# Kernel tuning notes

Measured on AMD Instinct MI355X. Metric: run time of the kernel, lower is better.

Reference implementation:

```python
import jax, jax.numpy as jnp
import numpy as np

H = 64
L = 3
NG = 1024
# node types: 0 user, 1 card, 2 transaction, 3 merchant, 4 location, 5 device
N_NODES = [100000, 150000, 500000, 20000, 5000, 50000]
N_TX = N_NODES[2]
FEAT_DIMS = [8, 6, 12, 6, 5, 5]
NAMES = ["user", "card", "transaction", "merchant", "location", "device"]
# relation r -> (src_type, dst_type); order matches the HeteroConv dict:
# owns, made, at, in, using, followed_by, owned_by, made_with, receives, has, used_in, preceded
REL = [(0, 1), (1, 2), (2, 3), (2, 4), (2, 5), (2, 2), (1, 0), (2, 1), (3, 2), (4, 2), (5, 2), (2, 2)]
E_CNT = [150000, 500000, 500000, 500000, 500000, 500000, 150000, 500000, 500000, 500000, 500000, 500000]


def gat_conv(x_src, x_dst, src, dst, W, a_s, a_d, b, n_dst):
    # PyG GATConv, heads=1, shared src/dst linear (int in_channels), no self-loops (bipartite hetero)
    xs = x_src @ W  # [Ns, H]
    xd = x_dst @ W  # [Nd, H]
    e = jax.nn.leaky_relu((xs @ a_s)[src] + (xd @ a_d)[dst], 0.2)  # [E]
    m = jax.ops.segment_max(e, dst, num_segments=n_dst)
    m = jnp.where(jnp.isfinite(m), m, 0.0)
    p = jnp.exp(e - m[dst])
    s = jax.ops.segment_sum(p, dst, num_segments=n_dst)
    alpha = p / (s[dst] + 1e-16)
    out = jax.ops.segment_sum(alpha[:, None] * xs[src], dst, num_segments=n_dst)
    return out + b


def setup_inputs():
    key = jax.random.key(0)
    ks = iter(jax.random.split(key, 80))
    inp = {}
    for n, d, nm in zip(N_NODES, FEAT_DIMS, NAMES):
        inp["x_" + nm] = jax.random.normal(next(ks), (n, d), jnp.float32)
    for d, nm in zip(FEAT_DIMS, NAMES):
        inp["emb_" + nm + "_W"] = (jax.random.normal(next(ks), (d, H), jnp.float32) / np.sqrt(d)).astype(jnp.float32)
        inp["emb_" + nm + "_b"] = jnp.zeros((H,), jnp.float32)
    inp["gat_W"] = (jax.random.normal(next(ks), (L, 12, H, H), jnp.float32) / np.sqrt(H)).astype(jnp.float32)
    inp["gat_a_src"] = jax.random.normal(next(ks), (L, 12, H), jnp.float32) * 0.1
    inp["gat_a_dst"] = jax.random.normal(next(ks), (L, 12, H), jnp.float32) * 0.1
    inp["gat_b"] = jnp.zeros((L, 12, H), jnp.float32)
    inp["pool_W"] = (jax.random.normal(next(ks), (2 * H, H), jnp.float32) / np.sqrt(2 * H)).astype(jnp.float32)
    inp["pool_b"] = jnp.zeros((H,), jnp.float32)
    inp["cls_W1"] = (jax.random.normal(next(ks), (H, H), jnp.float32) / np.sqrt(H)).astype(jnp.float32)
    inp["cls_b1"] = jnp.zeros((H,), jnp.float32)
    inp["cls_W2"] = (jax.random.normal(next(ks), (H, 1), jnp.float32) / np.sqrt(H)).astype(jnp.float32)
    inp["cls_b2"] = jnp.zeros((1,), jnp.float32)
    for r, (s, d) in enumerate(REL):
        inp[f"e{r}_src"] = jax.random.randint(next(ks), (E_CNT[r],), 0, N_NODES[s])
        inp[f"e{r}_dst"] = jax.random.randint(next(ks), (E_CNT[r],), 0, N_NODES[d])
    inp["batch"] = jnp.sort(jax.random.randint(next(ks), (N_TX,), 0, NG))
    return inp


def reference(x_user, x_card, x_transaction, x_merchant, x_location, x_device,
              emb_user_W, emb_user_b, emb_card_W, emb_card_b,
              emb_transaction_W, emb_transaction_b, emb_merchant_W, emb_merchant_b,
              emb_location_W, emb_location_b, emb_device_W, emb_device_b,
              gat_W, gat_a_src, gat_a_dst, gat_b,
              pool_W, pool_b, cls_W1, cls_b1, cls_W2, cls_b2,
              e0_src, e0_dst, e1_src, e1_dst, e2_src, e2_dst, e3_src, e3_dst,
              e4_src, e4_dst, e5_src, e5_dst, e6_src, e6_dst, e7_src, e7_dst,
              e8_src, e8_dst, e9_src, e9_dst, e10_src, e10_dst, e11_src, e11_dst,
              batch):
    edges = [(e0_src, e0_dst), (e1_src, e1_dst), (e2_src, e2_dst), (e3_src, e3_dst),
             (e4_src, e4_dst), (e5_src, e5_dst), (e6_src, e6_dst), (e7_src, e7_dst),
             (e8_src, e8_dst), (e9_src, e9_dst), (e10_src, e10_dst), (e11_src, e11_dst)]
    x = [x_user @ emb_user_W + emb_user_b,
         x_card @ emb_card_W + emb_card_b,
         x_transaction @ emb_transaction_W + emb_transaction_b,
         x_merchant @ emb_merchant_W + emb_merchant_b,
         x_location @ emb_location_W + emb_location_b,
         x_device @ emb_device_W + emb_device_b]
    for l in range(L):
        agg = [jnp.zeros((n, H), x[0].dtype) for n in N_NODES]
        for r, (s, d) in enumerate(REL):  # HeteroConv default aggr='sum'
            agg[d] = agg[d] + gat_conv(x[s], x[d], edges[r][0], edges[r][1],
                                       gat_W[l, r], gat_a_src[l, r], gat_a_dst[l, r],
                                       gat_b[l, r], N_NODES[d])
        x = [jax.nn.relu(a) for a in agg]  # dropout(p=0.2) is identity in eval mode
    tx = x[2]
    cnt = jax.ops.segment_sum(jnp.ones((N_TX,), tx.dtype), batch, num_segments=NG)
    mean_pool = jax.ops.segment_sum(tx, batch, num_segments=NG) / jnp.maximum(cnt, 1.0)[:, None]
    max_pool = jax.ops.segment_max(tx, batch, num_segments=NG)
    max_pool = jnp.where(jnp.isfinite(max_pool), max_pool, 0.0)
    pooled = jnp.concatenate([mean_pool, max_pool], axis=1) @ pool_W + pool_b
    h = jax.nn.relu(tx @ cls_W1 + cls_b1)
    fraud_scores = jax.nn.sigmoid(h @ cls_W2 + cls_b2)
    return fraud_scores, pooled
```

## Files before the change

### kernel.cpp

```cpp
#include <hip/hip_runtime.h>
#include <hip/hip_bf16.h>

typedef unsigned int u32;
typedef unsigned short u16;
typedef _Float16 f16;
typedef float f32x4 __attribute__((ext_vector_type(4)));
typedef short bf16x8 __attribute__((ext_vector_type(8)));

#define CDIV(a,b) (((a)+(b)-1)/(b))

__device__ __forceinline__ float bf2f(u32 h){ return __uint_as_float(h<<16); }
__device__ __forceinline__ u16 f2bf(float f){
  u32 u=__float_as_uint(f);
  return (u16)((u + 0x7fffu + ((u>>16)&1u))>>16);
}
__device__ __forceinline__ void unpack8(const u16* p, float* xr){
  uint4 v=*(const uint4*)p;
  xr[0]=bf2f(v.x&0xffffu); xr[1]=bf2f(v.x>>16);
  xr[2]=bf2f(v.y&0xffffu); xr[3]=bf2f(v.y>>16);
  xr[4]=bf2f(v.z&0xffffu); xr[5]=bf2f(v.z>>16);
  xr[6]=bf2f(v.w&0xffffu); xr[7]=bf2f(v.w>>16);
}
__device__ __forceinline__ int iclamp(int i, int n){
  unsigned u=(unsigned)i; return (u>=(unsigned)n)?0:i;
}

struct EdgeTab {
  const int* dst[12];
  const int* src[12];
  int seo[13];
  int rpo[13];
  int nd[12];
  int ns[12];
};

struct GTab {
  int nn[6]; int xo[6];
  int rst[12];
  int aso[12], ado[12], rpo[12], seo[12];
  int tord[6]; int bofs[7];
  int abofs[7];
  int nrel[6], rel[6][6];
  int nrole[6]; int rwv[6][12]; int rofs[6][12];
  int dszb;
};

__global__ void kdiag(float* out, int n, float v){
  int i=blockIdx.x*blockDim.x+threadIdx.x;
  if(i<n) out[i]=(i==0)?v:0.f;
}
__global__ void kzeroi(int* p, int n){
  int i=blockIdx.x*blockDim.x+threadIdx.x;
  if(i<n) p[i]=0;
}
__global__ void kbsum(const float* __restrict__ gb, float* __restrict__ bsum){
  int l=blockIdx.x/6, t=blockIdx.x%6, j=threadIdx.x;
  const int rd[12]={1,2,3,4,5,2,0,1,2,2,2,2};
  float a=0.f;
  #pragma unroll
  for(int r=0;r<12;++r) if(rd[r]==t) a += gb[(l*12+r)*64 + j];
  bsum[(l*6+t)*64 + j]=a;
}
__global__ void kwconv(const float* __restrict__ gw, u16* __restrict__ wt, int total){
  int o=blockIdx.x*blockDim.x+threadIdx.x;
  if(o>=total) return;
  int m=o>>12, rem=o&4095, j=rem>>6, k=rem&63;
  wt[o]=f2bf(gw[(m<<12)+(k<<6)+j]);
}
__global__ void kwv(const float* __restrict__ gw, const float* __restrict__ gas,
                    const float* __restrict__ gad, float* __restrict__ wv){
  int m=blockIdx.x;
  int lr=m>>1, role=m&1;
  int k=threadIdx.x;
  const float* a=(role?gad:gas)+(size_t)lr*64;
  const float* W=gw+(size_t)lr*4096;
  float acc=0.f;
  for(int j=0;j<64;++j) acc += W[k*64+j]*a[j];
  wv[(size_t)m*64+k]=acc;
}

__global__ void khistAll(EdgeTab et, int* __restrict__ RP, int Etot){
  int i=blockIdx.x*blockDim.x+threadIdx.x;
  if(i>=Etot) return;
  int r=0;
  #pragma unroll
  for(int k=1;k<12;++k) r += (i>=et.seo[k]) ? 1 : 0;
  int e=i-et.seo[r];
  int d=iclamp(et.dst[r][e], et.nd[r]);
  atomicAdd(RP+et.rpo[r]+d,1);
}
__global__ void kscan1(const int* __restrict__ hist, int* __restrict__ rp, int* __restrict__ bsum, int N){
  __shared__ int lds[256];
  __shared__ int pref[256];
  int b=blockIdx.x, t=threadIdx.x;
  int base=b*4096+t*16;
  int v[16]; int s=0;
  #pragma unroll
  for(int k=0;k<16;++k){ int idx=base+k; v[k]=(idx<N)?hist[idx]:0; s+=v[k]; }
  lds[t]=s; __syncthreads();
  if(t==0){ int run=0; for(int i=0;i<256;++i){ pref[i]=run; run+=lds[i]; } bsum[b]=run; }
  __syncthreads();
  int run=pref[t];
  #pragma unroll
  for(int k=0;k<16;++k){ int idx=base+k; if(idx<N) rp[idx]=run; run+=v[k]; }
}
__global__ void kscan2b(int* bsum, int nb){
  __shared__ int lds[256], pref[256], tot;
  int t=threadIdx.x;
  int v[4]; int s=0;
  #pragma unroll
  for(int k=0;k<4;++k){ int idx=t*4+k; v[k]=(idx<nb)?bsum[idx]:0; s+=v[k]; }
  lds[t]=s; __syncthreads();
  if(t==0){ int run=0; for(int i=0;i<256;++i){ pref[i]=run; run+=lds[i]; } tot=run; }
  __syncthreads();
  int run=pref[t];
  #pragma unroll
  for(int k=0;k<4;++k){ int idx=t*4+k; if(idx<nb){ int x=v[k]; bsum[idx]=run; run+=x; } }
  if(t==0) bsum[nb]=tot;
}
__global__ void kscan3(int* __restrict__ rp, const int* __restrict__ bsum, int N){
  int i=blockIdx.x*blockDim.x+threadIdx.x;
  if(i<N) rp[i]+=bsum[i>>12];
}
__global__ void kscatterAll(EdgeTab et, int* __restrict__ RP, int* __restrict__ SRCS, int Etot){
  int i=blockIdx.x*blockDim.x+threadIdx.x;
  if(i>=Etot) return;
  int r=0;
  #pragma unroll
  for(int k=1;k<12;++k) r += (i>=et.seo[k]) ? 1 : 0;
  int e=i-et.seo[r];
  int d=iclamp(et.dst[r][e], et.nd[r]);
  int pos=atomicAdd(RP+et.rpo[r]+d,1);
  SRCS[pos]=iclamp(et.src[r][e], et.ns[r]);
}

template<int D>
__global__ void kemb(const float* __restrict__ xin, const float* __restrict__ W,
                     const float* __restrict__ b, u16* __restrict__ xout, int N){
  int n=blockIdx.x*blockDim.x+threadIdx.x;
  if(n>=N) return;
  float xr[D];
  #pragma unroll
  for(int k=0;k<D;++k) xr[k]=xin[(long)n*D+k];
  u16* orow=xout+(long)n*64;
  for(int j0=0;j0<64;j0+=8){
    float acc[8];
    #pragma unroll
    for(int jj=0;jj<8;++jj){
      float a=b[j0+jj];
      #pragma unroll
      for(int k=0;k<D;++k) a += xr[k]*W[k*64+j0+jj];
      acc[jj]=a;
    }
    uint4 pk;
    pk.x=(u32)f2bf(acc[0])|((u32)f2bf(acc[1])<<16);
    pk.y=(u32)f2bf(acc[2])|((u32)f2bf(acc[3])<<16);
    pk.z=(u32)f2bf(acc[4])|((u32)f2bf(acc[5])<<16);
    pk.w=(u32)f2bf(acc[6])|((u32)f2bf(acc[7])<<16);
    *(uint4*)(orow+j0)=pk;
  }
}

__global__ void kalphaM(const u16* __restrict__ X, const float* __restrict__ WVl,
                        f16* __restrict__ AA, GTab tab){
  __shared__ float wv[12*64];
  int b=blockIdx.x, tid=threadIdx.x;
  int ti=0;
  #pragma unroll
  for(int k=1;k<6;++k) ti += (b>=tab.abofs[k]) ? 1 : 0;
  int t=tab.tord[ti];
  int nr=tab.nrole[t];
  for(int i=tid;i<nr*64;i+=256){
    int ro=i>>6, j=i&63;
    wv[i]=WVl[tab.rwv[t][ro]*64+j];
  }
  __syncthreads();
  int nid=(b-tab.abofs[ti])*256+tid;
  if(nid>=tab.nn[t]) return;
  const u16* row=X+((long)tab.xo[t]+nid)*64;
  float xr[64];
  #pragma unroll
  for(int j=0;j<64;j+=8) unpack8(row+j,xr+j);
  for(int ro=0;ro<nr;++ro){
    float acc=0.f;
    #pragma unroll
    for(int k=0;k<64;++k) acc += xr[k]*wv[ro*64+k];
    AA[tab.rofs[t][ro]+nid]=(f16)acc;
  }
}

#define LZ 0
#define LW 8192
#define LC 16384
__global__ void kfusedM2(const u16* __restrict__ Xc, u16* __restrict__ Xn,
                         const u16* __restrict__ WTl, const f16* __restrict__ AA,
                         const int* __restrict__ RP, const int* __restrict__ SRCS,
                         const float* __restrict__ BSl, GTab tab){
  __shared__ char L[32768];
  int tid=threadIdx.x;
  int b=blockIdx.x;
  int ti=0;
  #pragma unroll
  for(int k=1;k<6;++k) ti += (b>=tab.bofs[k]) ? 1 : 0;
  int t=tab.tord[ti];
  int d0=(b-tab.bofs[ti])*64;
  int Nt=tab.nn[t];
  int n=tid&63, q=tid>>6;
  int d=d0+n;

  f32x4 acc[4];
  #pragma unroll
  for(int ct=0;ct<4;++ct){ acc[ct][0]=0.f; acc[ct][1]=0.f; acc[ct][2]=0.f; acc[ct][3]=0.f; }

  int nrel=tab.nrel[t];
  for(int ri=0;ri<nrel;++ri){
    int r=tab.rel[t][ri];
    __syncthreads();
    {
      const uint4* s4=(const uint4*)(WTl+(size_t)r*4096);
      uint4 v0=s4[tid*2], v1=s4[tid*2+1];
      int b0=tid*32, j=b0>>7;
      *(uint4*)(L+LW+((b0   )^((j&7)<<4)))=v0;
      *(uint4*)(L+LW+((b0+16)^((j&7)<<4)))=v1;
    }
    float z[16];
    #pragma unroll
    for(int k=0;k<16;++k) z[k]=0.f;
    float sden=0.f;
    if(d<Nt){
      int b1=RP[tab.rpo[r]+d];
      int b0e= d? RP[tab.rpo[r]+d-1] : tab.seo[r];
      float adv=(float)AA[tab.dszb+tab.ado[r]+d];
      const u16* xbase=Xc+(long)tab.xo[tab.rst[r]]*64;
      const f16* asp=AA+tab.aso[r];
      float m=-3.4e38f;
      for(int e=b0e;e<b1;++e){
        int sr=SRCS[e];
        float ev=(float)asp[sr]+adv;
        ev = ev>=0.f?ev:0.2f*ev;
        float p;
        if(ev>m){
          float sc=__expf(m-ev);
          sden*=sc;
          #pragma unroll
          for(int k=0;k<16;++k) z[k]*=sc;
          m=ev; p=1.f;
        } else p=__expf(ev-m);
        sden+=p;
        const u16* rw=xbase+(long)sr*64+q*16;
        float xr[8];
        unpack8(rw,xr);
        #pragma unroll
        for(int k=0;k<8;++k) z[k]+=p*xr[k];
        unpack8(rw+8,xr);
        #pragma unroll
        for(int k=0;k<8;++k) z[8+k]+=p*xr[k];
      }
    }
    float inv=1.f/(sden+1e-16f);
    {
      uint4 p0,p1;
      p0.x=(u32)f2bf(z[0]*inv) |((u32)f2bf(z[1]*inv)<<16);
      p0.y=(u32)f2bf(z[2]*inv) |((u32)f2bf(z[3]*inv)<<16);
      p0.z=(u32)f2bf(z[4]*inv) |((u32)f2bf(z[5]*inv)<<16);
      p0.w=(u32)f2bf(z[6]*inv) |((u32)f2bf(z[7]*inv)<<16);
      p1.x=(u32)f2bf(z[8]*inv) |((u32)f2bf(z[9]*inv)<<16);
      p1.y=(u32)f2bf(z[10]*inv)|((u32)f2bf(z[11]*inv)<<16);
      p1.z=(u32)f2bf(z[12]*inv)|((u32)f2bf(z[13]*inv)<<16);
      p1.w=(u32)f2bf(z[14]*inv)|((u32)f2bf(z[15]*inv)<<16);
      int zb=n*128+q*32;
      *(uint4*)(L+LZ+((zb   )^((n&7)<<4)))=p0;
      *(uint4*)(L+LZ+((zb+16)^((n&7)<<4)))=p1;
    }
    __syncthreads();
    {
      int nt=q*16;
      int arow=nt+(n&15);
      int kb=(n>>4)*8;
      #pragma unroll
      for(int ks=0;ks<64;ks+=32){
        int ab=arow*128+(ks+kb)*2;
        uint4 av=*(uint4*)(L+LZ+(ab^((arow&7)<<4)));
        bf16x8 af=*(bf16x8*)&av;
        #pragma unroll
        for(int ct=0;ct<4;++ct){
          int jrow=ct*16+(n&15);
          int bb=jrow*128+(ks+kb)*2;
          uint4 bv=*(uint4*)(L+LW+(bb^((jrow&7)<<4)));
          bf16x8 bfr=*(bf16x8*)&bv;
          acc[ct]=__builtin_amdgcn_mfma_f32_16x16x32_bf16(af,bfr,acc[ct],0,0,0);
        }
      }
    }
  }
  {
    int nt=q*16;
    #pragma unroll
    for(int ct=0;ct<4;++ct){
      #pragma unroll
      for(int r4=0;r4<4;++r4){
        int crow=nt+(n>>4)*4+r4;
        int ccol=ct*16+(n&15);
        int cb=crow*256+ccol*4;
        *(float*)(L+LC+(cb^((crow&7)<<4)))=acc[ct][r4];
      }
    }
  }
  __syncthreads();
  {
    int nn=tid>>2, cq=tid&3;
    if(d0+nn<Nt){
      float cv[16];
      #pragma unroll
      for(int p=0;p<4;++p){
        int cb=nn*256+cq*64+p*16;
        uint4 v=*(uint4*)(L+LC+(cb^((nn&7)<<4)));
        const float* f=(const float*)&v;
        cv[p*4+0]=f[0]; cv[p*4+1]=f[1]; cv[p*4+2]=f[2]; cv[p*4+3]=f[3];
      }
      const float* bs=BSl+t*64+cq*16;
      u32 wd[8];
      #pragma unroll
      for(int i=0;i<8;++i){
        float lo=fmaxf(cv[2*i]  +bs[2*i],  0.f);
        float hi=fmaxf(cv[2*i+1]+bs[2*i+1],0.f);
        wd[i]=(u32)f2bf(lo)|((u32)f2bf(hi)<<16);
      }
      u16* orow=Xn+((long)tab.xo[t]+d0+nn)*64+cq*16;
      uint4 s0; s0.x=wd[0]; s0.y=wd[1]; s0.z=wd[2]; s0.w=wd[3];
      uint4 s1; s1.x=wd[4]; s1.y=wd[5]; s1.z=wd[6]; s1.w=wd[7];
      *(uint4*)orow=s0;
      *(uint4*)(orow+8)=s1;
    }
  }
}

__global__ void kcls(const u16* __restrict__ tx, const float* __restrict__ W1,
                     const float* __restrict__ b1, const float* __restrict__ W2,
                     const float* __restrict__ b2, float* __restrict__ out, int N){
  int n=blockIdx.x*blockDim.x+threadIdx.x;
  if(n>=N) return;
  const u16* row=tx+(long)n*64;
  float xr[64];
  #pragma unroll
  for(int j=0;j<64;j+=8) unpack8(row+j,xr+j);
  float acc2=0.f;
  for(int j=0;j<64;++j){
    float a=b1[j];
    #pragma unroll
    for(int k=0;k<64;++k) a += xr[k]*W1[k*64+j];
    a=fmaxf(a,0.f);
    acc2 += a*W2[j];
  }
  float zv=acc2+b2[0];
  out[n]=1.f/(1.f+__expf(-zv));
}

__global__ void kgrp(const int* __restrict__ batch, int* __restrict__ grp, int N){
  int g=blockIdx.x*blockDim.x+threadIdx.x;
  if(g>1024) return;
  if(g==1024){ grp[1024]=N; return; }
  int lo=0, hi=N;
  while(lo<hi){ int mid=(lo+hi)>>1; if(batch[mid]<g) lo=mid+1; else hi=mid; }
  grp[g]=lo;
}
__global__ void kpoolf(const u16* __restrict__ tx, const int* __restrict__ grp,
                       const float* __restrict__ pW, const float* __restrict__ pb,
                       float* __restrict__ out){
  __shared__ float S[256], M[256], V[128];
  int g=blockIdx.x, t=threadIdx.x, w=t>>6, j=t&63;
  int n0=grp[g], n1=grp[g+1];
  float s=0.f, m=-3.4e38f;
  for(int n=n0+w; n<n1; n+=4){
    float v=bf2f(tx[(long)n*64+j]);
    s+=v; m=fmaxf(m,v);
  }
  S[t]=s; M[t]=m; __syncthreads();
  if(t<64){
    float ss=S[t]+S[t+64]+S[t+128]+S[t+192];
    float mm=fmaxf(fmaxf(M[t],M[t+64]),fmaxf(M[t+128],M[t+192]));
    int cnt=n1-n0;
    V[t]=ss/fmaxf((float)cnt,1.f);
    V[64+t]=(cnt>0)?mm:0.f;
  }
  __syncthreads();
  if(t<64){
    float acc=pb[t];
    for(int k=0;k<128;++k) acc+=V[k]*pW[k*64+t];
    out[(long)g*64+t]=acc;
  }
}

extern "C" void kernel_launch(void* const* d_in, const int* in_sizes, int n_in,
                              void* d_out, int out_size, void* d_ws, size_t ws_size,
                              hipStream_t stream){
  const int   NN[6]={100000,150000,500000,20000,5000,50000};
  const long  XO[6]={0,100000,250000,750000,770000,775000};
  const int   RS[12]={0,1,2,2,2,2,1,2,3,4,5,2};
  const int   RD[12]={1,2,3,4,5,2,0,1,2,2,2,2};
  const int   EC[12]={150000,500000,500000,500000,500000,500000,150000,500000,500000,500000,500000,500000};

  const float* xin[6];  for(int t=0;t<6;++t) xin[t]=(const float*)d_in[t];
  const float* embW[6]; const float* embB[6];
  for(int t=0;t<6;++t){ embW[t]=(const float*)d_in[6+2*t]; embB[t]=(const float*)d_in[7+2*t]; }
  const float* gatW =(const float*)d_in[18];
  const float* gatAs=(const float*)d_in[19];
  const float* gatAd=(const float*)d_in[20];
  const float* gatB =(const float*)d_in[21];
  const float* poolW=(const float*)d_in[22];
  const float* poolB=(const float*)d_in[23];
  const float* W1=(const float*)d_in[24];
  const float* b1=(const float*)d_in[25];
  const float* W2=(const float*)d_in[26];
  const float* b2=(const float*)d_in[27];
  const int* esrc[12]; const int* edst[12];
  for(int r=0;r<12;++r){ esrc[r]=(const int*)d_in[28+2*r]; edst[r]=(const int*)d_in[29+2*r]; }
  const int* batch=(const int*)d_in[52];
  float* out=(float*)d_out;
  (void)in_sizes; (void)n_in;

  EdgeTab et;
  GTab tab;
  int rpo=0, seo=0, asz=0, dsz=0;
  for(int r=0;r<12;++r){
    et.dst[r]=edst[r]; et.src[r]=esrc[r];
    et.seo[r]=seo; et.rpo[r]=rpo;
    et.nd[r]=NN[RD[r]]; et.ns[r]=NN[RS[r]];
    tab.rst[r]=RS[r];
    tab.seo[r]=seo; tab.rpo[r]=rpo;
    tab.aso[r]=asz; tab.ado[r]=dsz;
    seo+=EC[r]; rpo+=NN[RD[r]]+1;
    asz+=NN[RS[r]]; dsz+=NN[RD[r]];
  }
  et.seo[12]=seo; et.rpo[12]=rpo;
  const int Etot=seo;
  const int RPtot=rpo;
  tab.dszb=asz;
  for(int t=0;t<6;++t){ tab.nn[t]=NN[t]; tab.xo[t]=(int)XO[t]; }
  const int TORD[6]={4,3,5,2,1,0};
  int bo=0, abo=0;
  for(int i=0;i<6;++i){
    int t=TORD[i];
    tab.tord[i]=t;
    tab.bofs[i]=bo;   bo+=CDIV(NN[t],64);
    tab.abofs[i]=abo; abo+=CDIV(NN[t],256);
  }
  tab.bofs[6]=bo; tab.abofs[6]=abo;
  for(int t=0;t<6;++t){ tab.nrel[t]=0; tab.nrole[t]=0; }
  for(int r=0;r<12;++r){
    int dt=RD[r];
    tab.rel[dt][tab.nrel[dt]++]=r;
    int st=RS[r];
    tab.rwv[st][tab.nrole[st]]=r*2+0;   tab.rofs[st][tab.nrole[st]++]=tab.aso[r];
    tab.rwv[dt][tab.nrole[dt]]=r*2+1;   tab.rofs[dt][tab.nrole[dt]++]=asz+tab.ado[r];
  }

  char* w=(char*)d_ws;
  size_t off=0;
  auto take=[&](size_t bytes)->void*{
    void* p=w+off; off+=(bytes+(size_t)255)&~(size_t)255; return p;
  };
  u16*   X1   =(u16*)  take(105600000);
  u16*   X2   =(u16*)  take(105600000);
  int*   RP   =(int*)  take((size_t)RPtot*4);
  int*   SRCS =(int*)  take((size_t)Etot*4);
  int*   BS   =(int*)  take(4096);
  f16*   AA   =(f16*)  take((size_t)(asz+dsz)*2);
  float* WV   =(float*)take(72*64*4);
  float* BSUM =(float*)take(4608);
  int*   GRP  =(int*)  take(4104);
  u16*   WT   =(u16*)  take(294912);
  size_t need=off;

  const int B=256;

  if(ws_size<need){
    kdiag<<<CDIV(out_size,B),B,0,stream>>>(out,out_size,(float)(ws_size>>20));
    return;
  }

  int nbs=CDIV(RPtot,4096);
  kzeroi<<<CDIV(RPtot,B),B,0,stream>>>(RP,RPtot);
  khistAll<<<CDIV(Etot,B),B,0,stream>>>(et,RP,Etot);
  kscan1<<<nbs,256,0,stream>>>(RP,RP,BS,RPtot);
  kscan2b<<<1,256,0,stream>>>(BS,nbs);
  kscan3<<<CDIV(RPtot,B),B,0,stream>>>(RP,BS,RPtot);
  kscatterAll<<<CDIV(Etot,B),B,0,stream>>>(et,RP,SRCS,Etot);

  kwconv<<<CDIV(147456,B),B,0,stream>>>(gatW,WT,147456);
  kwv<<<72,64,0,stream>>>(gatW,gatAs,gatAd,WV);
  kbsum<<<18,64,0,stream>>>(gatB,BSUM);

  kemb< 8><<<CDIV(NN[0],B),B,0,stream>>>(xin[0],embW[0],embB[0],X1+XO[0]*64,NN[0]);
  kemb< 6><<<CDIV(NN[1],B),B,0,stream>>>(xin[1],embW[1],embB[1],X1+XO[1]*64,NN[1]);
  kemb<12><<<CDIV(NN[2],B),B,0,stream>>>(xin[2],embW[2],embB[2],X1+XO[2]*64,NN[2]);
  kemb< 6><<<CDIV(NN[3],B),B,0,stream>>>(xin[3],embW[3],embB[3],X1+XO[3]*64,NN[3]);
  kemb< 5><<<CDIV(NN[4],B),B,0,stream>>>(xin[4],embW[4],embB[4],X1+XO[4]*64,NN[4]);
  kemb< 5><<<CDIV(NN[5],B),B,0,stream>>>(xin[5],embW[5],embB[5],X1+XO[5]*64,NN[5]);

  u16* Xc=X1; u16* Xn=X2;
  for(int l=0;l<3;++l){
    kalphaM<<<abo,256,0,stream>>>(Xc,WV+(size_t)l*1536,AA,tab);
    kfusedM2<<<bo,256,0,stream>>>(Xc,Xn,WT+(size_t)l*49152,AA,RP,SRCS,BSUM+(size_t)l*384,tab);
    u16* tmp=Xc; Xc=Xn; Xn=tmp;
  }

  kcls<<<CDIV(NN[2],B),B,0,stream>>>(Xc+XO[2]*64,W1,b1,W2,b2,out,NN[2]);

  kgrp<<<CDIV(1025,B),B,0,stream>>>(batch,GRP,NN[2]);
  kpoolf<<<1024,256,0,stream>>>(Xc+XO[2]*64,GRP,poolW,poolB,out+500000);
}
```

Measured before the change: 2.600 ms.

## Remap threads so four lanes share a node row; two-pass softmax; shrink LDS

```diff
diff --git a/kernel.cpp b/kernel.cpp
--- a/kernel.cpp
+++ b/kernel.cpp
@@ -191,12 +191,11 @@
 
 #define LZ 0
 #define LW 8192
-#define LC 16384
 __global__ void kfusedM2(const u16* __restrict__ Xc, u16* __restrict__ Xn,
                          const u16* __restrict__ WTl, const f16* __restrict__ AA,
                          const int* __restrict__ RP, const int* __restrict__ SRCS,
                          const float* __restrict__ BSl, GTab tab){
-  __shared__ char L[32768];
+  __shared__ char L[16384];
   int tid=threadIdx.x;
   int b=blockIdx.x;
   int ti=0;
@@ -205,8 +204,8 @@
   int t=tab.tord[ti];
   int d0=(b-tab.bofs[ti])*64;
   int Nt=tab.nn[t];
-  int n=tid&63, q=tid>>6;
-  int d=d0+n;
+  int nid=tid>>2, q=tid&3;
+  int d=d0+nid;
 
   f32x4 acc[4];
   #pragma unroll
@@ -235,26 +234,78 @@
       const f16* asp=AA+tab.aso[r];
       float m=-3.4e38f;
       for(int e=b0e;e<b1;++e){
-        int sr=SRCS[e];
-        float ev=(float)asp[sr]+adv;
+        float ev=(float)asp[SRCS[e]]+adv;
         ev = ev>=0.f?ev:0.2f*ev;
-        float p;
-        if(ev>m){
-          float sc=__expf(m-ev);
-          sden*=sc;
-          #pragma unroll
-          for(int k=0;k<16;++k) z[k]*=sc;
-          m=ev; p=1.f;
-        } else p=__expf(ev-m);
-        sden+=p;
-        const u16* rw=xbase+(long)sr*64+q*16;
+        m=fmaxf(m,ev);
+      }
+      int e=b0e;
+      for(; e+1<b1; e+=2){
+        int sr0=SRCS[e], sr1=SRCS[e+1];
+        float ev0=(float)asp[sr0]+adv; ev0 = ev0>=0.f?ev0:0.2f*ev0;
+        float ev1=(float)asp[sr1]+adv; ev1 = ev1>=0.f?ev1:0.2f*ev1;
+        float p0=__expf(ev0-m), p1=__expf(ev1-m);
+        uint4 v0=*(const uint4*)(xbase+(long)sr0*64+q*16);
+        uint4 v1=*(const uint4*)(xbase+(long)sr1*64+q*16);
+        sden+=p0+p1;
         float xr[8];
-        unpack8(rw,xr);
-        #pragma unroll
-        for(int k=0;k<8;++k) z[k]+=p*xr[k];
-        unpack8(rw+8,xr);
-        #pragma unroll
-        for(int k=0;k<8;++k) z[8+k]+=p*xr[k];
+        unpack8((const u16*)&v0,xr);
+        #pragma unroll
+        for(int k=0;k<8;++k) z[k]+=p0*xr[k];
+        { uint2 hi; hi.x=v0.z; hi.y=v0.w;
+          float xh[4];
+          xh[0]=bf2f(hi.x&0xffffu); xh[1]=bf2f(hi.x>>16);
+          xh[2]=bf2f(hi.y&0xffffu); xh[3]=bf2f(hi.y>>16);
+          (void)xh;
+        }
+        unpack8((const u16*)&v1,xr);
+        #pragma unroll
+        for(int k=0;k<8;++k) z[8+k]+=0.f;
+        (void)p1;
+      }
+      #pragma unroll
+      for(int k=0;k<16;++k) z[k]=0.f;
+      sden=0.f;
+      for(e=b0e; e+1<b1; e+=2){
+        int sr0=SRCS[e], sr1=SRCS[e+1];
+        float ev0=(float)asp[sr0]+adv; ev0 = ev0>=0.f?ev0:0.2f*ev0;
+        float ev1=(float)asp[sr1]+adv; ev1 = ev1>=0.f?ev1:0.2f*ev1;
+        float p0=__expf(ev0-m), p1=__expf(ev1-m);
+        const u16* rw0=xbase+(long)sr0*64+q*16;
+        const u16* rw1=xbase+(long)sr1*64+q*16;
+        uint4 a0=*(const uint4*)rw0;
+        uint4 a1=*(const uint4*)(rw0+8);
+        uint4 c0=*(const uint4*)rw1;
+        uint4 c1=*(const uint4*)(rw1+8);
+        sden+=p0+p1;
+        float xr[8];
+        unpack8((const u16*)&a0,xr);
+        #pragma unroll
+        for(int k=0;k<8;++k) z[k]+=p0*xr[k];
+        unpack8((const u16*)&a1,xr);
+        #pragma unroll
+        for(int k=0;k<8;++k) z[8+k]+=p0*xr[k];
+        unpack8((const u16*)&c0,xr);
+        #pragma unroll
+        for(int k=0;k<8;++k) z[k]+=p1*xr[k];
+        unpack8((const u16*)&c1,xr);
+        #pragma unroll
+        for(int k=0;k<8;++k) z[8+k]+=p1*xr[k];
+      }
+      if(e<b1){
+        int sr0=SRCS[e];
+        float ev0=(float)asp[sr0]+adv; ev0 = ev0>=0.f?ev0:0.2f*ev0;
+        float p0=__expf(ev0-m);
+        const u16* rw0=xbase+(long)sr0*64+q*16;
+        uint4 a0=*(const uint4*)rw0;
+        uint4 a1=*(const uint4*)(rw0+8);
+        sden+=p0;
+        float xr[8];
+        unpack8((const u16*)&a0,xr);
+        #pragma unroll
+        for(int k=0;k<8;++k) z[k]+=p0*xr[k];
+        unpack8((const u16*)&a1,xr);
+        #pragma unroll
+        for(int k=0;k<8;++k) z[8+k]+=p0*xr[k];
       }
     }
     float inv=1.f/(sden+1e-16f);
@@ -268,15 +319,16 @@
       p1.y=(u32)f2bf(z[10]*inv)|((u32)f2bf(z[11]*inv)<<16);
       p1.z=(u32)f2bf(z[12]*inv)|((u32)f2bf(z[13]*inv)<<16);
       p1.w=(u32)f2bf(z[14]*inv)|((u32)f2bf(z[15]*inv)<<16);
-      int zb=n*128+q*32;
-      *(uint4*)(L+LZ+((zb   )^((n&7)<<4)))=p0;
-      *(uint4*)(L+LZ+((zb+16)^((n&7)<<4)))=p1;
+      int zb=nid*128+q*32;
+      *(uint4*)(L+LZ+((zb   )^((nid&7)<<4)))=p0;
+      *(uint4*)(L+LZ+((zb+16)^((nid&7)<<4)))=p1;
     }
     __syncthreads();
     {
-      int nt=q*16;
-      int arow=nt+(n&15);
-      int kb=(n>>4)*8;
+      int w=tid>>6, l=tid&63;
+      int nt=w*16;
+      int arow=nt+(l&15);
+      int kb=(l>>4)*8;
       #pragma unroll
       for(int ks=0;ks<64;ks+=32){
         int ab=arow*128+(ks+kb)*2;
@@ -284,7 +336,7 @@
         bf16x8 af=*(bf16x8*)&av;
         #pragma unroll
         for(int ct=0;ct<4;++ct){
-          int jrow=ct*16+(n&15);
+          int jrow=ct*16+(l&15);
           int bb=jrow*128+(ks+kb)*2;
           uint4 bv=*(uint4*)(L+LW+(bb^((jrow&7)<<4)));
           bf16x8 bfr=*(bf16x8*)&bv;
@@ -293,16 +345,18 @@
       }
     }
   }
+  __syncthreads();
   {
-    int nt=q*16;
+    int w=tid>>6, l=tid&63;
+    int nt=w*16;
     #pragma unroll
     for(int ct=0;ct<4;++ct){
       #pragma unroll
       for(int r4=0;r4<4;++r4){
-        int crow=nt+(n>>4)*4+r4;
-        int ccol=ct*16+(n&15);
+        int crow=nt+(l>>4)*4+r4;
+        int ccol=ct*16+(l&15);
         int cb=crow*256+ccol*4;
-        *(float*)(L+LC+(cb^((crow&7)<<4)))=acc[ct][r4];
+        *(float*)(L+(cb^((crow&7)<<4)))=acc[ct][r4];
       }
     }
   }
@@ -314,7 +368,7 @@
       #pragma unroll
       for(int p=0;p<4;++p){
         int cb=nn*256+cq*64+p*16;
-        uint4 v=*(uint4*)(L+LC+(cb^((nn&7)<<4)));
+        uint4 v=*(uint4*)(L+(cb^((nn&7)<<4)));
         const float* f=(const float*)&v;
         cv[p*4+0]=f[0]; cv[p*4+1]=f[1]; cv[p*4+2]=f[2]; cv[p*4+3]=f[3];
       }
```

New measurement: 2.491 ms. -4.2%, faster.
